# Optimization experiments

Hardware: AMD Instinct MI355X
Metric: run time of the kernel (lower is better)

The kernel has to match this reference:

```python
import jax, jax.numpy as jnp
import numpy as np

NUM_HEADS = 12


def setup_inputs() -> dict:
    key = jax.random.key(0)
    k1, k2, k3, k4, k5 = jax.random.split(key, 5)
    B, N, C = 4, 1024, 768
    x = jax.random.normal(k1, (B, N, C), dtype=jnp.float32)
    y = jax.random.normal(k2, (B, N, C), dtype=jnp.float32)
    w_qkv = jax.random.normal(k3, (4 * C, C), dtype=jnp.float32) * 0.02
    w_proj = jax.random.normal(k4, (C, C), dtype=jnp.float32) * 0.02
    b_proj = jax.random.normal(k5, (C,), dtype=jnp.float32) * 0.02
    return {"x": x, "y": y, "w_qkv": w_qkv, "w_proj": w_proj, "b_proj": b_proj}


def reference(x, y, w_qkv, w_proj, b_proj):
    B, N, C = x.shape
    H = NUM_HEADS
    hd = C // H
    scale = hd ** (-0.5)

    def qkv4(t):
        # Linear(dim, 4*dim, bias=False): t @ W^T -> [B,N,4C] -> [4,B,H,N,hd]
        p = (t @ w_qkv.T).reshape(B, N, 4, H, hd).transpose(2, 0, 3, 1, 4)
        return p[0], p[1], p[2], p[3]

    qxo, qx, kx, vx = qkv4(x)
    qyo, qy, ky, _vy_from_y = qkv4(y)
    vy = vx  # faithful to source: vy = qkv[3] (from x), not qkv2[3]

    def attend(q, k, v, neg):
        s = jnp.einsum('bhnd,bhmd->bhnm', q, k) * scale
        a = jax.nn.softmax(-s if neg else s, axis=-1)
        o = jnp.einsum('bhnm,bhmd->bhnd', a, v)
        return o.transpose(0, 2, 1, 3).reshape(B, N, C)

    x_self = attend(qx, kx, vx, False)
    y_self = attend(qy, ky, vy, False)
    x_cross = attend(qyo, kx, vx, True)   # attnx = -(qyo @ kx^T)
    y_cross = attend(qxo, ky, vy, True)   # attny = -(qxo @ ky^T)

    out_x = (x_self + x_cross) @ w_proj.T + b_proj
    out_y = (y_self + y_cross) @ w_proj.T + b_proj
    return (out_x, out_y)
```

## Files before the change

### kernel.cpp

```cpp
#include <hip/hip_runtime.h>
#include <hip/hip_bf16.h>
#include <stdint.h>


#define BB 4
#define NN 1024
#define CC 768
#define HH 12
#define HD 64

typedef unsigned short u16;
typedef short short8 __attribute__((ext_vector_type(8)));
typedef float f32x4 __attribute__((ext_vector_type(4)));

extern "C" __device__ float __ocml_native_exp2_f32(float);

__device__ __forceinline__ u16 f2bf(float f) {
  unsigned int u = __float_as_uint(f);
  return (u16)((u + 0x7fffu + ((u >> 16) & 1u)) >> 16);
}

__device__ __forceinline__ void load_lds16(const u16* g, u16* l) {
  __builtin_amdgcn_global_load_lds((__attribute__((address_space(1))) const void*)g,
                                   (__attribute__((address_space(3))) void*)l, 16, 0, 0);
}

__global__ __launch_bounds__(256)
void cvt_bf16(const float* __restrict__ x, const float* __restrict__ y,
              const float* __restrict__ wq, const float* __restrict__ wp,
              u16* __restrict__ xb, u16* __restrict__ yb,
              u16* __restrict__ wqb, u16* __restrict__ wpb)
{
  const int seg = blockIdx.y;
  const float* src = seg == 0 ? x : (seg == 1 ? y : (seg == 2 ? wq : wp));
  u16* dst = seg == 0 ? xb : (seg == 1 ? yb : (seg == 2 ? wqb : wpb));
  const int n = (seg == 3) ? 768 * 768 : ((seg == 2) ? 3072 * 768 : 4096 * 768);
  const int i = (blockIdx.x * 256 + threadIdx.x) * 8;
  if (i >= n) return;
  float sc = 1.0f;
  if (seg == 2) {
    const int row = i / 768;
    sc = (row < 768) ? -0.18033688f : (row < 1536 ? 0.18033688f : 1.0f);
  }
  float4 a = *(const float4*)(src + i);
  float4 b = *(const float4*)(src + i + 4);
  ushort4 u0 = {f2bf(a.x * sc), f2bf(a.y * sc), f2bf(a.z * sc), f2bf(a.w * sc)};
  ushort4 u1 = {f2bf(b.x * sc), f2bf(b.y * sc), f2bf(b.z * sc), f2bf(b.w * sc)};
  *(ushort4*)(dst + i) = u0;
  *(ushort4*)(dst + i + 4) = u1;
}

__global__ __launch_bounds__(256)
void vtrans(const u16* __restrict__ qkvx, u16* __restrict__ VT)
{
  const int blk = blockIdx.x;
  const int xcd = blk & 7, slot = blk >> 3;
  const int bh = (slot >> 5) * 8 + xcd;
  const int kt = slot & 31;
  const int b = bh / HH, h = bh % HH;
  const int t = threadIdx.x;
  const int key = kt * 32 + (t >> 3), d0 = (t & 7) * 8;
  uint4 v = *(const uint4*)(qkvx + (size_t)(b * NN + key) * 3072 + 3 * CC + h * HD + d0);
  u16 e[8];
  *(uint4*)e = v;
#pragma unroll
  for (int i = 0; i < 8; i++)
    VT[(size_t)(bh * 64 + d0 + i) * 1024 + key] = e[i];
}

template<int NP, bool BF16OUT, bool BIAS>
__global__ __launch_bounds__(256)
void gemm_mfma(const u16* __restrict__ A0, const u16* __restrict__ A1,
               const u16* __restrict__ W, const float* __restrict__ bias,
               void* __restrict__ C0, void* __restrict__ C1)
{
  __shared__ u16 As[128 * 64];
  __shared__ u16 Bs[128 * 64];
  const u16* A = blockIdx.z ? A1 : A0;
  void* C = blockIdx.z ? C1 : C0;
  const int m0 = blockIdx.y * 128, n0 = blockIdx.x * 128;
  const int t = threadIdx.x, w = t >> 6, lane = t & 63;
  const int c = lane & 15, qq = lane >> 4;
  const int mq = (w >> 1) * 64, nq = (w & 1) * 64;

  const int lrow = lane >> 3;
  const int lchunk = (lane & 7) ^ lrow;
  size_t arow[4], brow[4];
#pragma unroll
  for (int i = 0; i < 4; i++) {
    const int r = (w * 4 + i) * 8 + lrow;
    arow[i] = (size_t)(m0 + r) * 768 + lchunk * 8;
    brow[i] = (size_t)(n0 + r) * 768 + lchunk * 8;
  }

  f32x4 acc[4][4] = {};
  for (int k0 = 0; k0 < 768; k0 += 64) {
    __syncthreads();
#pragma unroll
    for (int i = 0; i < 4; i++) {
      load_lds16(A + arow[i] + k0, As + (w * 4 + i) * 512);
      load_lds16(W + brow[i] + k0, Bs + (w * 4 + i) * 512);
    }
    __syncthreads();
#pragma unroll
    for (int s = 0; s < 2; s++) {
      const int swz = ((s * 4 + qq) ^ (c & 7)) * 8;
      short8 af[4], bf[4];
#pragma unroll
      for (int i = 0; i < 4; i++)
        af[i] = *(const short8*)&As[(mq + i * 16 + c) * 64 + swz];
#pragma unroll
      for (int j = 0; j < 4; j++)
        bf[j] = *(const short8*)&Bs[(nq + j * 16 + c) * 64 + swz];
#pragma unroll
      for (int i = 0; i < 4; i++)
#pragma unroll
        for (int j = 0; j < 4; j++)
          acc[i][j] = __builtin_amdgcn_mfma_f32_16x16x32_bf16(af[i], bf[j], acc[i][j], 0, 0, 0);
    }
  }
  float bj[4] = {0.f, 0.f, 0.f, 0.f};
  if (BIAS) {
#pragma unroll
    for (int j = 0; j < 4; j++) bj[j] = bias[n0 + nq + c + j * 16];
  }
#pragma unroll
  for (int i = 0; i < 4; i++)
#pragma unroll
    for (int r = 0; r < 4; r++) {
      const size_t row = (size_t)(m0 + mq + i * 16 + qq * 4 + r) * NP + n0 + nq + c;
      if (BF16OUT) {
#pragma unroll
        for (int j = 0; j < 4; j++)
          ((u16*)C)[row + j * 16] = f2bf(acc[i][j][r]);
      } else {
#pragma unroll
        for (int j = 0; j < 4; j++)
          ((float*)C)[row + j * 16] = acc[i][j][r] + bj[j];
      }
    }
}

__global__ __launch_bounds__(256, 3)
void attn_pair_mfma(const u16* __restrict__ qkvx, const u16* __restrict__ qkvy,
                    const u16* __restrict__ VT,
                    u16* __restrict__ sum_x, u16* __restrict__ sum_y)
{
  __shared__ __align__(16) u16 smem[25600];
  float (*Of)[68] = (float(*)[68])smem;

  const int blk = blockIdx.x;
  const int xcd = blk & 7, slot = blk >> 3;
  const int bh = (slot >> 5) * 8 + xcd;
  const int inner = slot & 31;
  const int qt = inner >> 1, pair = inner & 1;
  const int b = bh / HH, head = bh % HH;
  const u16* q1 = pair ? qkvy : qkvx;
  const u16* q2 = pair ? qkvx : qkvy;
  const u16* ks = pair ? qkvy : qkvx;
  u16* outp = pair ? sum_y : sum_x;

  const int t = threadIdx.x, w = t >> 6, lane = t & 63;
  const int c = lane & 15, qq = lane >> 4;

  short8 Qf[2][2];
  {
    const int qrow = qt * 64 + w * 16 + c;
    const u16* qs = q1 + (size_t)(b * NN + qrow) * 3072 + CC + head * HD + qq * 8;
    const u16* qc = q2 + (size_t)(b * NN + qrow) * 3072 + head * HD + qq * 8;
    Qf[0][0] = *(const short8*)qs;
    Qf[0][1] = *(const short8*)(qs + 32);
    Qf[1][0] = *(const short8*)qc;
    Qf[1][1] = *(const short8*)(qc + 32);
  }

  const u16* kbase = ks + (size_t)(b * NN) * 3072 + 2 * CC + head * HD;
  const u16* vtb = VT + (size_t)(bh * 64) * 1024;

  const int lr = lane >> 3;
  const int sc8 = ((lane & 7) ^ lr) * 8;

  u16* Pw = smem + 16384 + w * 2304;

  short8 ones;
#pragma unroll
  for (int i = 0; i < 8; i++) ones[i] = (short)0x3F80;

  f32x4 O[2][4] = {};
  f32x4 L[2] = {};

  const int cx = c & 7;
  const int koff0 = (qq ^ cx) * 8;
  const int koff1 = ((4 + qq) ^ cx) * 8;
  const int c6 = (6 * c) & 7;
  const int poff0 = ((qq + c6) & 7) * 8;
  const int poff1 = ((4 + qq + c6) & 7) * 8;

#pragma unroll
  for (int i = 0; i < 2; i++) {
    const int r = (2 * w + i) * 8 + lr;
    load_lds16(kbase + (size_t)r * 3072 + sc8, smem + (2 * w + i) * 512);
    load_lds16(vtb + (size_t)r * 1024 + sc8, smem + 8192 + (2 * w + i) * 512);
  }
  __syncthreads();

  for (int c16 = 0; c16 < 16; ++c16) {
    const int cur = c16 & 1;
    const u16* Kb = smem + cur * 4096;
    const u16* Vb = smem + 8192 + cur * 4096;

    if (c16 < 15) {
      u16* Kn = smem + (cur ^ 1) * 4096;
      u16* Vn = smem + 8192 + (cur ^ 1) * 4096;
#pragma unroll
      for (int i = 0; i < 2; i++) {
        const int r = (2 * w + i) * 8 + lr;
        load_lds16(kbase + (size_t)((c16 + 1) * 64 + r) * 3072 + sc8,
                   Kn + (2 * w + i) * 512);
        load_lds16(vtb + (size_t)r * 1024 + (c16 + 1) * 64 + sc8,
                   Vn + (2 * w + i) * 512);
      }
    }

#pragma unroll
    for (int t4 = 0; t4 < 4; t4++) {
      const u16* kr = Kb + (16 * t4 + c) * 64;
      short8 k0 = *(const short8*)(kr + koff0);
      short8 k1 = *(const short8*)(kr + koff1);
      const int l = 2 * t4 + (qq >> 1);
      const int base = c * 72 + (((l + c6) & 7) * 8) + 4 * (qq & 1);
#pragma unroll
      for (int s = 0; s < 2; s++) {
        f32x4 z = {0.f, 0.f, 0.f, 0.f};
        z = __builtin_amdgcn_mfma_f32_16x16x32_bf16(k0, Qf[s][0], z, 0, 0, 0);
        z = __builtin_amdgcn_mfma_f32_16x16x32_bf16(k1, Qf[s][1], z, 0, 0, 0);
        unsigned int u0 = __float_as_uint(__ocml_native_exp2_f32(z[0]));
        unsigned int u1 = __float_as_uint(__ocml_native_exp2_f32(z[1]));
        unsigned int u2 = __float_as_uint(__ocml_native_exp2_f32(z[2]));
        unsigned int u3 = __float_as_uint(__ocml_native_exp2_f32(z[3]));
        uint2 pk;
        pk.x = __builtin_amdgcn_perm(u1, u0, 0x07060302u);
        pk.y = __builtin_amdgcn_perm(u3, u2, 0x07060302u);
        *(uint2*)(Pw + s * 1152 + base) = pk;
      }
    }

    short8 pa[2][2];
#pragma unroll
    for (int s = 0; s < 2; s++) {
      const u16* pr = Pw + s * 1152 + c * 72;
      pa[s][0] = *(const short8*)(pr + poff0);
      pa[s][1] = *(const short8*)(pr + poff1);
      L[s] = __builtin_amdgcn_mfma_f32_16x16x32_bf16(pa[s][0], ones, L[s], 0, 0, 0);
      L[s] = __builtin_amdgcn_mfma_f32_16x16x32_bf16(pa[s][1], ones, L[s], 0, 0, 0);
    }
#pragma unroll
    for (int t4 = 0; t4 < 4; t4++) {
      const u16* vr = Vb + (16 * t4 + c) * 64;
      short8 v0 = *(const short8*)(vr + koff0);
      short8 v1 = *(const short8*)(vr + koff1);
#pragma unroll
      for (int s = 0; s < 2; s++) {
        O[s][t4] = __builtin_amdgcn_mfma_f32_16x16x32_bf16(pa[s][0], v0, O[s][t4], 0, 0, 0);
        O[s][t4] = __builtin_amdgcn_mfma_f32_16x16x32_bf16(pa[s][1], v1, O[s][t4], 0, 0, 0);
      }
    }

    __syncthreads();
  }

  float is[4], ic[4];
#pragma unroll
  for (int r = 0; r < 4; r++) {
    is[r] = 1.0f / L[0][r];
    ic[r] = 1.0f / L[1][r];
  }
#pragma unroll
  for (int t4 = 0; t4 < 4; t4++)
#pragma unroll
    for (int r = 0; r < 4; r++)
      Of[w * 16 + 4 * qq + r][16 * t4 + c] =
          O[0][t4][r] * is[r] + O[1][t4][r] * ic[r];
  __syncthreads();
#pragma unroll
  for (int p = 0; p < 4; p++) {
    const int idx = p * 256 + t;
    const int row = idx >> 4, c4 = (idx & 15) * 4;
    float4 v = *(const float4*)&Of[row][c4];
    ushort4 u = {f2bf(v.x), f2bf(v.y), f2bf(v.z), f2bf(v.w)};
    *(ushort4*)(outp + (size_t)(b * NN + qt * 64 + row) * CC + head * HD + c4) = u;
  }
}

extern "C" void kernel_launch(void* const* d_in, const int* in_sizes, int n_in,
                              void* d_out, int out_size, void* d_ws, size_t ws_size,
                              hipStream_t stream)
{
  const float* x      = (const float*)d_in[0];
  const float* y      = (const float*)d_in[1];
  const float* w_qkv  = (const float*)d_in[2];
  const float* w_proj = (const float*)d_in[3];
  const float* b_proj = (const float*)d_in[4];

  u16* qkv_x = (u16*)d_ws;
  u16* qkv_y = qkv_x + (size_t)4096 * 3072;
  u16* rest = qkv_y + (size_t)4096 * 3072;
  u16* sum_x = rest;
  u16* sum_y = sum_x + (size_t)4096 * 768;
  u16* x_bf  = rest;
  u16* y_bf  = x_bf + (size_t)4096 * 768;
  u16* wq_bf = y_bf + (size_t)4096 * 768;
  u16* wp_bf = wq_bf + (size_t)3072 * 768;
  u16* VT    = wp_bf + (size_t)768 * 768;
  float* out_x = (float*)d_out;
  float* out_y = out_x + (size_t)4096 * 768;

  cvt_bf16<<<dim3(1536, 4), 256, 0, stream>>>(x, y, w_qkv, w_proj,
                                              x_bf, y_bf, wq_bf, wp_bf);

  gemm_mfma<3072, true, false><<<dim3(24, 32, 2), 256, 0, stream>>>(
      x_bf, y_bf, wq_bf, nullptr, qkv_x, qkv_y);

  vtrans<<<dim3(1536), 256, 0, stream>>>(qkv_x, VT);

  attn_pair_mfma<<<dim3(1536), 256, 0, stream>>>(qkv_x, qkv_y, VT, sum_x, sum_y);

  gemm_mfma<768, false, true><<<dim3(6, 32, 2), 256, 0, stream>>>(
      sum_x, sum_y, wp_bf, b_proj, out_x, out_y);
}
```

Before: 214.3 us.

## Switch attention to 32x32 MFMA with register-resident P and skip unused V GEMM

The attention kernel now uses 32x32x16 bf16 MFMA tiles. Each wave covers 32 queries and half of each 64-key chunk. The softmax probabilities are repacked in registers with v_permlane32_swap instead of going through LDS. Row sums are taken with VALU adds and combined across waves through LDS at the end. This removes the per-wave P scratch buffer and the ones-matrix MFMA, which cuts LDS traffic and LDS usage, and occupancy bounds drop from 3 to 2. Separately, the QKV GEMM skips the V columns for the y input, since vy is taken from x, which removes a quarter of that GEMM's work for y.

```diff
diff --git a/kernel.cpp b/kernel.cpp
--- a/kernel.cpp
+++ b/kernel.cpp
@@ -12,6 +12,7 @@
 typedef unsigned short u16;
 typedef short short8 __attribute__((ext_vector_type(8)));
 typedef float f32x4 __attribute__((ext_vector_type(4)));
+typedef float f32x16 __attribute__((ext_vector_type(16)));
 
 extern "C" __device__ float __ocml_native_exp2_f32(float);
 
@@ -23,6 +24,14 @@
 __device__ __forceinline__ void load_lds16(const u16* g, u16* l) {
   __builtin_amdgcn_global_load_lds((__attribute__((address_space(1))) const void*)g,
                                    (__attribute__((address_space(3))) void*)l, 16, 0, 0);
+}
+
+__device__ __forceinline__ void pl32swap(unsigned& a, unsigned& b) {
+  asm("v_permlane32_swap_b32 %0, %1" : "+v"(a), "+v"(b));
+}
+
+__device__ __forceinline__ unsigned pack_hi(float e0, float e1) {
+  return __builtin_amdgcn_perm(__float_as_uint(e1), __float_as_uint(e0), 0x07060302u);
 }
 
 __global__ __launch_bounds__(256)
@@ -68,7 +77,7 @@
     VT[(size_t)(bh * 64 + d0 + i) * 1024 + key] = e[i];
 }
 
-template<int NP, bool BF16OUT, bool BIAS>
+template<int NP, bool BF16OUT, bool BIAS, int NZ1>
 __global__ __launch_bounds__(256)
 void gemm_mfma(const u16* __restrict__ A0, const u16* __restrict__ A1,
                const u16* __restrict__ W, const float* __restrict__ bias,
@@ -76,9 +85,10 @@
 {
   __shared__ u16 As[128 * 64];
   __shared__ u16 Bs[128 * 64];
+  const int m0 = blockIdx.y * 128, n0 = blockIdx.x * 128;
+  if (blockIdx.z && n0 >= NZ1) return;
   const u16* A = blockIdx.z ? A1 : A0;
   void* C = blockIdx.z ? C1 : C0;
-  const int m0 = blockIdx.y * 128, n0 = blockIdx.x * 128;
   const int t = threadIdx.x, w = t >> 6, lane = t & 63;
   const int c = lane & 15, qq = lane >> 4;
   const int mq = (w >> 1) * 64, nq = (w & 1) * 64;
@@ -141,13 +151,14 @@
     }
 }
 
-__global__ __launch_bounds__(256, 3)
+__global__ __launch_bounds__(256, 2)
 void attn_pair_mfma(const u16* __restrict__ qkvx, const u16* __restrict__ qkvy,
                     const u16* __restrict__ VT,
                     u16* __restrict__ sum_x, u16* __restrict__ sum_y)
 {
-  __shared__ __align__(16) u16 smem[25600];
+  __shared__ __align__(16) u16 smem[16384];
   float (*Of)[68] = (float(*)[68])smem;
+  float* LfB = (float*)(smem + 8704);
 
   const int blk = blockIdx.x;
   const int xcd = blk & 7, slot = blk >> 3;
@@ -161,17 +172,19 @@
   u16* outp = pair ? sum_y : sum_x;
 
   const int t = threadIdx.x, w = t >> 6, lane = t & 63;
-  const int c = lane & 15, qq = lane >> 4;
-
-  short8 Qf[2][2];
+  const int qh = w >> 1, kh = w & 1;
+  const int c31 = lane & 31, h = lane >> 5;
+
+  short8 Qf[2][4];
   {
-    const int qrow = qt * 64 + w * 16 + c;
-    const u16* qs = q1 + (size_t)(b * NN + qrow) * 3072 + CC + head * HD + qq * 8;
-    const u16* qc = q2 + (size_t)(b * NN + qrow) * 3072 + head * HD + qq * 8;
-    Qf[0][0] = *(const short8*)qs;
-    Qf[0][1] = *(const short8*)(qs + 32);
-    Qf[1][0] = *(const short8*)qc;
-    Qf[1][1] = *(const short8*)(qc + 32);
+    const int qrow = qt * 64 + qh * 32 + c31;
+    const u16* qs = q1 + (size_t)(b * NN + qrow) * 3072 + CC + head * HD + 8 * h;
+    const u16* qc = q2 + (size_t)(b * NN + qrow) * 3072 + head * HD + 8 * h;
+#pragma unroll
+    for (int cc = 0; cc < 4; cc++) {
+      Qf[0][cc] = *(const short8*)(qs + 16 * cc);
+      Qf[1][cc] = *(const short8*)(qc + 16 * cc);
+    }
   }
 
   const u16* kbase = ks + (size_t)(b * NN) * 3072 + 2 * CC + head * HD;
@@ -179,22 +192,10 @@
 
   const int lr = lane >> 3;
   const int sc8 = ((lane & 7) ^ lr) * 8;
-
-  u16* Pw = smem + 16384 + w * 2304;
-
-  short8 ones;
-#pragma unroll
-  for (int i = 0; i < 8; i++) ones[i] = (short)0x3F80;
-
-  f32x4 O[2][4] = {};
-  f32x4 L[2] = {};
-
-  const int cx = c & 7;
-  const int koff0 = (qq ^ cx) * 8;
-  const int koff1 = ((4 + qq) ^ cx) * 8;
-  const int c6 = (6 * c) & 7;
-  const int poff0 = ((qq + c6) & 7) * 8;
-  const int poff1 = ((4 + qq + c6) & 7) * 8;
+  const int x7 = c31 & 7;
+
+  f32x16 O[2][2] = {};
+  float Lh[2] = {0.f, 0.f};
 
 #pragma unroll
   for (int i = 0; i < 2; i++) {
@@ -222,65 +223,98 @@
       }
     }
 
-#pragma unroll
-    for (int t4 = 0; t4 < 4; t4++) {
-      const u16* kr = Kb + (16 * t4 + c) * 64;
-      short8 k0 = *(const short8*)(kr + koff0);
-      short8 k1 = *(const short8*)(kr + koff1);
-      const int l = 2 * t4 + (qq >> 1);
-      const int base = c * 72 + (((l + c6) & 7) * 8) + 4 * (qq & 1);
-#pragma unroll
-      for (int s = 0; s < 2; s++) {
-        f32x4 z = {0.f, 0.f, 0.f, 0.f};
-        z = __builtin_amdgcn_mfma_f32_16x16x32_bf16(k0, Qf[s][0], z, 0, 0, 0);
-        z = __builtin_amdgcn_mfma_f32_16x16x32_bf16(k1, Qf[s][1], z, 0, 0, 0);
-        unsigned int u0 = __float_as_uint(__ocml_native_exp2_f32(z[0]));
-        unsigned int u1 = __float_as_uint(__ocml_native_exp2_f32(z[1]));
-        unsigned int u2 = __float_as_uint(__ocml_native_exp2_f32(z[2]));
-        unsigned int u3 = __float_as_uint(__ocml_native_exp2_f32(z[3]));
-        uint2 pk;
-        pk.x = __builtin_amdgcn_perm(u1, u0, 0x07060302u);
-        pk.y = __builtin_amdgcn_perm(u3, u2, 0x07060302u);
-        *(uint2*)(Pw + s * 1152 + base) = pk;
-      }
-    }
-
-    short8 pa[2][2];
+    short8 kf[4];
+#pragma unroll
+    for (int cc = 0; cc < 4; cc++)
+      kf[cc] = *(const short8*)(Kb + (kh * 32 + c31) * 64 + (((2 * cc + h) ^ x7) * 8));
+    short8 vf[2][2];
+#pragma unroll
+    for (int dc = 0; dc < 2; dc++)
+#pragma unroll
+      for (int kc = 0; kc < 2; kc++)
+        vf[dc][kc] = *(const short8*)(Vb + (dc * 32 + c31) * 64 +
+                                      (((4 * kh + 2 * kc + h) ^ x7) * 8));
+
 #pragma unroll
     for (int s = 0; s < 2; s++) {
-      const u16* pr = Pw + s * 1152 + c * 72;
-      pa[s][0] = *(const short8*)(pr + poff0);
-      pa[s][1] = *(const short8*)(pr + poff1);
-      L[s] = __builtin_amdgcn_mfma_f32_16x16x32_bf16(pa[s][0], ones, L[s], 0, 0, 0);
-      L[s] = __builtin_amdgcn_mfma_f32_16x16x32_bf16(pa[s][1], ones, L[s], 0, 0, 0);
-    }
-#pragma unroll
-    for (int t4 = 0; t4 < 4; t4++) {
-      const u16* vr = Vb + (16 * t4 + c) * 64;
-      short8 v0 = *(const short8*)(vr + koff0);
-      short8 v1 = *(const short8*)(vr + koff1);
-#pragma unroll
-      for (int s = 0; s < 2; s++) {
-        O[s][t4] = __builtin_amdgcn_mfma_f32_16x16x32_bf16(pa[s][0], v0, O[s][t4], 0, 0, 0);
-        O[s][t4] = __builtin_amdgcn_mfma_f32_16x16x32_bf16(pa[s][1], v1, O[s][t4], 0, 0, 0);
+      f32x16 z = {0.f, 0.f, 0.f, 0.f, 0.f, 0.f, 0.f, 0.f,
+                  0.f, 0.f, 0.f, 0.f, 0.f, 0.f, 0.f, 0.f};
+#pragma unroll
+      for (int cc = 0; cc < 4; cc++)
+        z = __builtin_amdgcn_mfma_f32_32x32x16_bf16(kf[cc], Qf[s][cc], z, 0, 0, 0);
+
+      float e[16];
+#pragma unroll
+      for (int r = 0; r < 16; r++) {
+        float v = __ocml_native_exp2_f32(z[r]);
+        e[r] = __uint_as_float(__float_as_uint(v) & 0xFFFF0000u);
+      }
+      Lh[s] += ((((e[0] + e[1]) + (e[2] + e[3])) + ((e[4] + e[5]) + (e[6] + e[7]))) +
+                (((e[8] + e[9]) + (e[10] + e[11])) + ((e[12] + e[13]) + (e[14] + e[15]))));
+
+      unsigned pk[4][2];
+#pragma unroll
+      for (int g = 0; g < 4; g++) {
+        pk[g][0] = pack_hi(e[4 * g + 0], e[4 * g + 1]);
+        pk[g][1] = pack_hi(e[4 * g + 2], e[4 * g + 3]);
+      }
+      unsigned a00 = pk[0][0], a20 = pk[1][0]; pl32swap(a00, a20);
+      unsigned a10 = pk[0][1], a30 = pk[1][1]; pl32swap(a10, a30);
+      unsigned a01 = pk[2][0], a21 = pk[3][0]; pl32swap(a01, a21);
+      unsigned a11 = pk[2][1], a31 = pk[3][1]; pl32swap(a11, a31);
+      union { unsigned u[4]; short8 s8; } pa0, pa1;
+      pa0.u[0] = a00; pa0.u[1] = a10; pa0.u[2] = a20; pa0.u[3] = a30;
+      pa1.u[0] = a01; pa1.u[1] = a11; pa1.u[2] = a21; pa1.u[3] = a31;
+
+#pragma unroll
+      for (int dc = 0; dc < 2; dc++) {
+        O[s][dc] = __builtin_amdgcn_mfma_f32_32x32x16_bf16(pa0.s8, vf[dc][0], O[s][dc], 0, 0, 0);
+        O[s][dc] = __builtin_amdgcn_mfma_f32_32x32x16_bf16(pa1.s8, vf[dc][1], O[s][dc], 0, 0, 0);
       }
     }
 
     __syncthreads();
   }
 
-  float is[4], ic[4];
-#pragma unroll
-  for (int r = 0; r < 4; r++) {
-    is[r] = 1.0f / L[0][r];
-    ic[r] = 1.0f / L[1][r];
-  }
-#pragma unroll
-  for (int t4 = 0; t4 < 4; t4++)
-#pragma unroll
-    for (int r = 0; r < 4; r++)
-      Of[w * 16 + 4 * qq + r][16 * t4 + c] =
-          O[0][t4][r] * is[r] + O[1][t4][r] * ic[r];
+  float Lw[2];
+#pragma unroll
+  for (int s = 0; s < 2; s++) {
+    unsigned ua = __float_as_uint(Lh[s]), ub = __float_as_uint(Lh[s]);
+    pl32swap(ua, ub);
+    Lw[s] = __uint_as_float(ua) + __uint_as_float(ub);
+  }
+  if (lane < 32) {
+    LfB[0 + kh * 64 + qh * 32 + lane] = Lw[0];
+    LfB[128 + kh * 64 + qh * 32 + lane] = Lw[1];
+  }
+  __syncthreads();
+
+  float oc[2][16];
+#pragma unroll
+  for (int r = 0; r < 16; r++) {
+    const int q = qh * 32 + (r & 3) + 8 * (r >> 2) + 4 * h;
+    const float iL0 = 1.0f / (LfB[q] + LfB[64 + q]);
+    const float iL1 = 1.0f / (LfB[128 + q] + LfB[192 + q]);
+    oc[0][r] = O[0][0][r] * iL0 + O[1][0][r] * iL1;
+    oc[1][r] = O[0][1][r] * iL0 + O[1][1][r] * iL1;
+  }
+  if (kh == 0) {
+#pragma unroll
+    for (int r = 0; r < 16; r++) {
+      const int q = qh * 32 + (r & 3) + 8 * (r >> 2) + 4 * h;
+      Of[q][c31] = oc[0][r];
+      Of[q][32 + c31] = oc[1][r];
+    }
+  }
+  __syncthreads();
+  if (kh == 1) {
+#pragma unroll
+    for (int r = 0; r < 16; r++) {
+      const int q = qh * 32 + (r & 3) + 8 * (r >> 2) + 4 * h;
+      Of[q][c31] += oc[0][r];
+      Of[q][32 + c31] += oc[1][r];
+    }
+  }
   __syncthreads();
 #pragma unroll
   for (int p = 0; p < 4; p++) {
@@ -318,13 +352,13 @@
   cvt_bf16<<<dim3(1536, 4), 256, 0, stream>>>(x, y, w_qkv, w_proj,
                                               x_bf, y_bf, wq_bf, wp_bf);
 
-  gemm_mfma<3072, true, false><<<dim3(24, 32, 2), 256, 0, stream>>>(
+  gemm_mfma<3072, true, false, 2304><<<dim3(24, 32, 2), 256, 0, stream>>>(
       x_bf, y_bf, wq_bf, nullptr, qkv_x, qkv_y);
 
   vtrans<<<dim3(1536), 256, 0, stream>>>(qkv_x, VT);
 
   attn_pair_mfma<<<dim3(1536), 256, 0, stream>>>(qkv_x, qkv_y, VT, sum_x, sum_y);
 
-  gemm_mfma<768, false, true><<<dim3(6, 32, 2), 256, 0, stream>>>(
+  gemm_mfma<768, false, true, 768><<<dim3(6, 32, 2), 256, 0, stream>>>(
       sum_x, sum_y, wp_bf, b_proj, out_x, out_y);
 }
```

Measured after the change: 227.7 us. 1.06x slower.
